# Kernel tuning notes

Measured on AMD Instinct MI355X. Metric: run time of the kernel, lower is better.

Reference implementation:

```python
import jax, jax.numpy as jnp
import numpy as np

SR_S = 4  # search_range_spatial
SR_D = 2  # search_range_depth


def setup_inputs() -> dict:
    key = jax.random.key(0)
    k1, k2, k3, k4 = jax.random.split(key, 4)
    b, c, h, w, d = 1, 32, 80, 80, 20
    return {
        'mpi1_features': jax.random.normal(k1, (b, c, h, w, d), jnp.float32),
        'mpi1_alpha': jax.random.uniform(k3, (b, 1, h, w, d), jnp.float32),
        'mpi2_features': jax.random.normal(k2, (b, c, h, w, d), jnp.float32),
        'mpi2_alpha': jax.random.uniform(k4, (b, 1, h, w, d), jnp.float32),
    }


def _correlation(mpi1_features, mpi1_alpha, mpi2_features, mpi2_alpha):
    so = 2 * SR_S + 1  # spatial_output_dim = 9
    do = 2 * SR_D + 1  # depth_output_dim = 5
    b, c, h, w, d = mpi1_features.shape
    ca = mpi1_alpha.shape[1]
    # visibility masks: any alpha along depth -> clip to [0,1], broadcast over depth
    mask1 = jnp.clip(jnp.sum(mpi1_alpha, axis=-1, keepdims=True), 0.0, 1.0)
    mask2 = jnp.clip(jnp.sum(mpi2_alpha, axis=-1, keepdims=True), 0.0, 1.0)
    mask1 = jnp.broadcast_to(mask1, mpi1_alpha.shape)
    mask2 = jnp.broadcast_to(mask2, mpi1_alpha.shape)
    pad = ((0, 0), (0, 0), (SR_S, SR_S), (SR_S, SR_S), (SR_D, SR_D))
    f2p = jnp.pad(mpi2_features, pad)                      # zeros, like F.pad default
    m2p = jnp.pad(mask2, pad, constant_values=1.0)         # mask padded with 1
    # displacement grid in torch loop order: k (depth) outer, then i, then j
    kk, ii, jj = jnp.meshgrid(jnp.arange(do), jnp.arange(so), jnp.arange(so), indexing='ij')
    disp = jnp.stack([ii.ravel(), jj.ravel(), kk.ravel()], axis=1)  # [D, 3]

    def step(carry, ijk):
        i, j, k = ijk[0], ijk[1], ijk[2]
        f2s = jax.lax.dynamic_slice(f2p, (0, 0, i, j, k), (b, c, h, w, d))
        m2s = jax.lax.dynamic_slice(m2p, (0, 0, i, j, k), (b, ca, h, w, d))
        cost = jnp.mean(mpi1_features * f2s, axis=1)                 # [b,h,w,d]
        cm = jnp.clip(jnp.sum(mask1 * m2s, axis=1), 0.0, 1.0)        # [b,h,w,d]
        return carry, (cost, cm)

    _, (cv, cvm) = jax.lax.scan(step, None, disp)
    # [D,b,h,w,d] -> [b,D,h,w,d]  (D = do*so*so = 405 channels, torch cat order)
    cost_volume = jnp.moveaxis(cv, 0, 1)
    cost_volume_mask = jnp.moveaxis(cvm, 0, 1)
    return cost_volume, cost_volume_mask


def reference(mpi1_features, mpi1_alpha, mpi2_features, mpi2_alpha):
    return _correlation(mpi1_features, mpi1_alpha, mpi2_features, mpi2_alpha)
```

## Files before the change

### kernel.cpp

```cpp
#include <hip/hip_runtime.h>

#define H 80
#define W 80
#define DD 20
#define C 32
#define NPOS (H*W)
#define NP3 (NPOS*DD)
#define SO 9
#define DO_ 5
#define NDISP (DO_*SO*SO)

#define NC 4
#define NCHUNK (C/NC)
#define XQ 20
#define COLS 28
#define ZST 28
#define F2S_FLOATS (NC*COLS*ZST)

__global__ __launch_bounds__(320)
void fused_kernel(const float* __restrict__ f1, const float* __restrict__ a1,
                  const float* __restrict__ f2, const float* __restrict__ a2,
                  float* __restrict__ outc, float* __restrict__ outm)
{
    __shared__ __align__(16) float f2s[F2S_FLOATS];
    __shared__ float m1s[XQ];
    __shared__ float m2s[COLS];

    int bid = blockIdx.x;
    int swz = (bid & 7) * 360 + (bid >> 3);
    int y  = swz / 36;
    int r0 = swz % 36;
    int di = r0 >> 2;
    int xq = r0 & 3;

    int t   = threadIdx.x;
    int djg = t / 100;
    int r   = t % 100;
    int xl  = r / 5;
    int zg  = r % 5;
    int z0  = zg * 4;
    int x   = xq * XQ + xl;
    int pos = y * W + x;
    int y2  = y + di - 4;
    bool y2ok = ((unsigned)y2 < (unsigned)H);
    bool act  = (t < 300);

    for (int i = t; i < F2S_FLOATS / 4; i += 320)
        ((float4*)f2s)[i] = make_float4(0.f, 0.f, 0.f, 0.f);

    if (t < XQ){
        const float* p = a1 + (y * W + xq * XQ + t) * DD;
        float s = 0.f;
        #pragma unroll
        for (int q = 0; q < 5; ++q){
            float4 v = *(const float4*)(p + q * 4);
            s += v.x + v.y + v.z + v.w;
        }
        m1s[t] = fminf(fmaxf(s, 0.f), 1.f);
    } else if (t >= 32 && t < 32 + COLS){
        int col = t - 32;
        int x2 = xq * XQ + col - 4;
        float m = 1.f;
        if (y2ok && ((unsigned)x2 < (unsigned)W)){
            const float* p = a2 + (y2 * W + x2) * DD;
            float s = 0.f;
            #pragma unroll
            for (int q = 0; q < 5; ++q){
                float4 v = *(const float4*)(p + q * 4);
                s += v.x + v.y + v.z + v.w;
            }
            m = fminf(fmaxf(s, 0.f), 1.f);
        }
        m2s[col] = m;
    }
    __syncthreads();

    float acc[3][DO_][4];
    #pragma unroll
    for (int i = 0; i < 3; ++i)
        #pragma unroll
        for (int j = 0; j < DO_; ++j)
            #pragma unroll
            for (int k = 0; k < 4; ++k) acc[i][j][k] = 0.f;

    const float* a_base = f1 + pos * DD + z0;

    #pragma unroll 1
    for (int cc = 0; cc < NCHUNK; ++cc){
        if (y2ok && t < NC * COLS){
            int c   = t / COLS;
            int col = t % COLS;
            int x2  = xq * XQ + col - 4;
            if ((unsigned)x2 < (unsigned)W){
                const float* p = f2 + (size_t)(cc * NC + c) * NP3 + (y2 * W + x2) * DD;
                float* d = f2s + (c * COLS + col) * ZST + 2;
                #pragma unroll
                for (int q = 0; q < 5; ++q){
                    float4 v = *(const float4*)(p + q * 4);
                    *(float2*)(d + q * 4)     = make_float2(v.x, v.y);
                    *(float2*)(d + q * 4 + 2) = make_float2(v.z, v.w);
                }
            }
        }
        float av[NC][4];
        if (act){
            #pragma unroll
            for (int c = 0; c < NC; ++c){
                float4 v = *(const float4*)(a_base + (size_t)(cc * NC + c) * NP3);
                av[c][0] = v.x; av[c][1] = v.y; av[c][2] = v.z; av[c][3] = v.w;
            }
        }
        __syncthreads();
        if (act){
            #pragma unroll
            for (int c = 0; c < NC; ++c){
                #pragma unroll
                for (int djl = 0; djl < 3; ++djl){
                    int dj = djg * 3 + djl;
                    const float* bp = f2s + (c * COLS + xl + dj) * ZST + z0;
                    float4 b0 = *(const float4*)(bp);
                    float4 b1 = *(const float4*)(bp + 4);
                    float bb[8] = {b0.x, b0.y, b0.z, b0.w, b1.x, b1.y, b1.z, b1.w};
                    #pragma unroll
                    for (int dk = 0; dk < DO_; ++dk)
                        #pragma unroll
                        for (int z = 0; z < 4; ++z)
                            acc[djl][dk][z] = fmaf(av[c][z], bb[z + dk], acc[djl][dk][z]);
                }
            }
        }
        __syncthreads();
    }

    if (act){
        const float sc = 1.0f / 32.0f;
        float m1v = m1s[xl];
        #pragma unroll
        for (int djl = 0; djl < 3; ++djl){
            int dj = djg * 3 + djl;
            float m2v = m2s[xl + dj];
            float mi = fminf(m1v * m2v, 1.f);
            #pragma unroll
            for (int dk = 0; dk < DO_; ++dk){
                size_t off = (size_t)(dk * 81 + di * 9 + dj) * NP3 + pos * DD + z0;
                float4 wv;
                wv.x = acc[djl][dk][0] * sc;
                wv.y = acc[djl][dk][1] * sc;
                wv.z = acc[djl][dk][2] * sc;
                wv.w = acc[djl][dk][3] * sc;
                *(float4*)(outc + off) = wv;
                int zlo = 2 - dk, zhi = 22 - dk;
                float4 mv;
                mv.x = (z0 + 0 >= zlo && z0 + 0 < zhi) ? mi : m1v;
                mv.y = (z0 + 1 >= zlo && z0 + 1 < zhi) ? mi : m1v;
                mv.z = (z0 + 2 >= zlo && z0 + 2 < zhi) ? mi : m1v;
                mv.w = (z0 + 3 >= zlo && z0 + 3 < zhi) ? mi : m1v;
                *(float4*)(outm + off) = mv;
            }
        }
    }
}

extern "C" void kernel_launch(void* const* d_in, const int* in_sizes, int n_in,
                              void* d_out, int out_size, void* d_ws, size_t ws_size,
                              hipStream_t stream)
{
    const float* f1 = (const float*)d_in[0];
    const float* a1 = (const float*)d_in[1];
    const float* f2 = (const float*)d_in[2];
    const float* a2 = (const float*)d_in[3];
    float* outc = (float*)d_out;
    float* outm = outc + (size_t)NDISP * NP3;
    (void)d_ws; (void)ws_size; (void)in_sizes; (void)n_in;

    fused_kernel<<<80 * SO * 4, 320, 0, stream>>>(f1, a1, f2, a2, outc, outm);
}
```

Measured before the change: 514.9 us.

## Double-buffer f2 shared tiles, widen channel chunk, use nontemporal output stores

```diff
diff --git a/kernel.cpp b/kernel.cpp
--- a/kernel.cpp
+++ b/kernel.cpp
@@ -10,19 +10,21 @@
 #define DO_ 5
 #define NDISP (DO_*SO*SO)
 
-#define NC 4
+#define NC 8
 #define NCHUNK (C/NC)
 #define XQ 20
 #define COLS 28
 #define ZST 28
-#define F2S_FLOATS (NC*COLS*ZST)
+#define CHUNK_FLOATS (NC*COLS*ZST)
 
-__global__ __launch_bounds__(320)
+typedef float nt4 __attribute__((ext_vector_type(4)));
+
+__global__ __launch_bounds__(320, 4)
 void fused_kernel(const float* __restrict__ f1, const float* __restrict__ a1,
                   const float* __restrict__ f2, const float* __restrict__ a2,
                   float* __restrict__ outc, float* __restrict__ outm)
 {
-    __shared__ __align__(16) float f2s[F2S_FLOATS];
+    __shared__ __align__(16) float f2s[2][CHUNK_FLOATS];
     __shared__ float m1s[XQ];
     __shared__ float m2s[COLS];
 
@@ -45,33 +47,51 @@
     bool y2ok = ((unsigned)y2 < (unsigned)H);
     bool act  = (t < 300);
 
-    for (int i = t; i < F2S_FLOATS / 4; i += 320)
+    int s    = t - 96;
+    int sc_  = s / COLS;
+    int scol = s % COLS;
+    int sx2  = xq * XQ + scol - 4;
+    bool stager = (t >= 96) && y2ok && ((unsigned)sx2 < (unsigned)W);
+    const float* sp_base = stager ? (f2 + (size_t)sc_ * NP3 + (y2 * W + sx2) * DD) : f2;
+    float* sd = &f2s[0][0] + (sc_ * COLS + scol) * ZST + 2;
+
+    for (int i = t; i < 2 * CHUNK_FLOATS / 4; i += 320)
         ((float4*)f2s)[i] = make_float4(0.f, 0.f, 0.f, 0.f);
 
     if (t < XQ){
         const float* p = a1 + (y * W + xq * XQ + t) * DD;
-        float s = 0.f;
+        float sm = 0.f;
         #pragma unroll
         for (int q = 0; q < 5; ++q){
             float4 v = *(const float4*)(p + q * 4);
-            s += v.x + v.y + v.z + v.w;
+            sm += v.x + v.y + v.z + v.w;
         }
-        m1s[t] = fminf(fmaxf(s, 0.f), 1.f);
+        m1s[t] = fminf(fmaxf(sm, 0.f), 1.f);
     } else if (t >= 32 && t < 32 + COLS){
         int col = t - 32;
         int x2 = xq * XQ + col - 4;
         float m = 1.f;
         if (y2ok && ((unsigned)x2 < (unsigned)W)){
             const float* p = a2 + (y2 * W + x2) * DD;
-            float s = 0.f;
+            float sm = 0.f;
             #pragma unroll
             for (int q = 0; q < 5; ++q){
                 float4 v = *(const float4*)(p + q * 4);
-                s += v.x + v.y + v.z + v.w;
+                sm += v.x + v.y + v.z + v.w;
             }
-            m = fminf(fmaxf(s, 0.f), 1.f);
+            m = fminf(fmaxf(sm, 0.f), 1.f);
         }
         m2s[col] = m;
+    }
+    __syncthreads();
+
+    if (stager){
+        #pragma unroll
+        for (int q = 0; q < 5; ++q){
+            float4 v = *(const float4*)(sp_base + q * 4);
+            *(float2*)(sd + q * 4)     = make_float2(v.x, v.y);
+            *(float2*)(sd + q * 4 + 2) = make_float2(v.z, v.w);
+        }
     }
     __syncthreads();
 
@@ -87,37 +107,26 @@
 
     #pragma unroll 1
     for (int cc = 0; cc < NCHUNK; ++cc){
-        if (y2ok && t < NC * COLS){
-            int c   = t / COLS;
-            int col = t % COLS;
-            int x2  = xq * XQ + col - 4;
-            if ((unsigned)x2 < (unsigned)W){
-                const float* p = f2 + (size_t)(cc * NC + c) * NP3 + (y2 * W + x2) * DD;
-                float* d = f2s + (c * COLS + col) * ZST + 2;
-                #pragma unroll
-                for (int q = 0; q < 5; ++q){
-                    float4 v = *(const float4*)(p + q * 4);
-                    *(float2*)(d + q * 4)     = make_float2(v.x, v.y);
-                    *(float2*)(d + q * 4 + 2) = make_float2(v.z, v.w);
-                }
+        if (cc < NCHUNK - 1 && stager){
+            const float* p = sp_base + (size_t)(cc + 1) * NC * NP3;
+            float* d = sd + ((cc + 1) & 1) * CHUNK_FLOATS;
+            #pragma unroll
+            for (int q = 0; q < 5; ++q){
+                float4 v = *(const float4*)(p + q * 4);
+                *(float2*)(d + q * 4)     = make_float2(v.x, v.y);
+                *(float2*)(d + q * 4 + 2) = make_float2(v.z, v.w);
             }
         }
-        float av[NC][4];
         if (act){
+            const float* base = &f2s[cc & 1][0];
             #pragma unroll
             for (int c = 0; c < NC; ++c){
-                float4 v = *(const float4*)(a_base + (size_t)(cc * NC + c) * NP3);
-                av[c][0] = v.x; av[c][1] = v.y; av[c][2] = v.z; av[c][3] = v.w;
-            }
-        }
-        __syncthreads();
-        if (act){
-            #pragma unroll
-            for (int c = 0; c < NC; ++c){
+                float4 avv = *(const float4*)(a_base + (size_t)(cc * NC + c) * NP3);
+                float av[4] = {avv.x, avv.y, avv.z, avv.w};
                 #pragma unroll
                 for (int djl = 0; djl < 3; ++djl){
                     int dj = djg * 3 + djl;
-                    const float* bp = f2s + (c * COLS + xl + dj) * ZST + z0;
+                    const float* bp = base + (c * COLS + xl + dj) * ZST + z0;
                     float4 b0 = *(const float4*)(bp);
                     float4 b1 = *(const float4*)(bp + 4);
                     float bb[8] = {b0.x, b0.y, b0.z, b0.w, b1.x, b1.y, b1.z, b1.w};
@@ -125,11 +134,11 @@
                     for (int dk = 0; dk < DO_; ++dk)
                         #pragma unroll
                         for (int z = 0; z < 4; ++z)
-                            acc[djl][dk][z] = fmaf(av[c][z], bb[z + dk], acc[djl][dk][z]);
+                            acc[djl][dk][z] = fmaf(av[z], bb[z + dk], acc[djl][dk][z]);
                 }
             }
         }
-        __syncthreads();
+        if (cc < NCHUNK - 1) __syncthreads();
     }
 
     if (act){
@@ -143,19 +152,19 @@
             #pragma unroll
             for (int dk = 0; dk < DO_; ++dk){
                 size_t off = (size_t)(dk * 81 + di * 9 + dj) * NP3 + pos * DD + z0;
-                float4 wv;
+                nt4 wv;
                 wv.x = acc[djl][dk][0] * sc;
                 wv.y = acc[djl][dk][1] * sc;
                 wv.z = acc[djl][dk][2] * sc;
                 wv.w = acc[djl][dk][3] * sc;
-                *(float4*)(outc + off) = wv;
+                __builtin_nontemporal_store(wv, (nt4*)(outc + off));
                 int zlo = 2 - dk, zhi = 22 - dk;
-                float4 mv;
+                nt4 mv;
                 mv.x = (z0 + 0 >= zlo && z0 + 0 < zhi) ? mi : m1v;
                 mv.y = (z0 + 1 >= zlo && z0 + 1 < zhi) ? mi : m1v;
                 mv.z = (z0 + 2 >= zlo && z0 + 2 < zhi) ? mi : m1v;
                 mv.w = (z0 + 3 >= zlo && z0 + 3 < zhi) ? mi : m1v;
-                *(float4*)(outm + off) = mv;
+                __builtin_nontemporal_store(mv, (nt4*)(outm + off));
             }
         }
     }
```

Measured after the change: 576.7 us. 1.12x slower.
